# Kernel tuning notes

Measured on AMD Instinct MI355X. Metric: run time of the kernel, lower is better.

The kernel has to match this reference:

```python
import jax, jax.numpy as jnp
import numpy as np

B, S, D = 4, 1024, 1024
H = 16
DK = D // H  # 64
F = 4096
EPS = 1e-6


def layer_norm(x, gamma, beta):
    mu = jnp.mean(x, axis=-1, keepdims=True)
    var = jnp.mean(jnp.square(x - mu), axis=-1, keepdims=True)
    return (x - mu) * jax.lax.rsqrt(var + EPS) * gamma + beta


def setup_inputs() -> dict:
    key = jax.random.key(0)
    ks = jax.random.split(key, 16)
    sd = 0.02
    return {
        "x": jax.random.normal(ks[0], (B, S, D), dtype=jnp.float32),
        "Wq": jax.random.normal(ks[1], (H, D, DK), dtype=jnp.float32) * sd,
        "bq": jnp.zeros((H, DK), dtype=jnp.float32),
        "Wk": jax.random.normal(ks[2], (H, D, DK), dtype=jnp.float32) * sd,
        "bk": jnp.zeros((H, DK), dtype=jnp.float32),
        "Wv": jax.random.normal(ks[3], (H, D, DK), dtype=jnp.float32) * sd,
        "bv": jnp.zeros((H, DK), dtype=jnp.float32),
        "Wo": jax.random.normal(ks[4], (D, D), dtype=jnp.float32) * sd,
        "bo": jnp.zeros((D,), dtype=jnp.float32),
        "W1": jax.random.normal(ks[5], (D, F), dtype=jnp.float32) * sd,
        "b1": jnp.zeros((F,), dtype=jnp.float32),
        "W2": jax.random.normal(ks[6], (F, D), dtype=jnp.float32) * sd,
        "b2": jnp.zeros((D,), dtype=jnp.float32),
        "g1": jnp.ones((D,), dtype=jnp.float32),
        "be1": jnp.zeros((D,), dtype=jnp.float32),
        "g2": jnp.ones((D,), dtype=jnp.float32),
        "be2": jnp.zeros((D,), dtype=jnp.float32),
    }


def reference(x, Wq, bq, Wk, bk, Wv, bv, Wo, bo, W1, b1, W2, b2, g1, be1, g2, be2):
    # Per-head Dense projections, expressed as one batched einsum.
    # q/k/v: [B, H, S, DK]
    q = jnp.einsum('bsd,hdk->bhsk', x, Wq) + bq[:, None, :]
    k = jnp.einsum('bsd,hdk->bhsk', x, Wk) + bk[:, None, :]
    v = jnp.einsum('bsd,hdk->bhsk', x, Wv) + bv[:, None, :]
    scale = 1.0 / jnp.sqrt(jnp.float32(DK))
    scores = jnp.einsum('bhqk,bhsk->bhqs', q, k) * scale  # [B,H,S,S]
    attn = jax.nn.softmax(scores, axis=-1)
    ctx = jnp.einsum('bhqs,bhsk->bhqk', attn, v)  # [B,H,S,DK]
    # concat heads along last dim -> [B,S,D]
    ctx = jnp.transpose(ctx, (0, 2, 1, 3)).reshape(B, S, D)
    mh = ctx @ Wo + bo
    # dropout is identity at inference
    h1 = layer_norm(mh + x, g1, be1)
    ffn = jax.nn.relu(h1 @ W1 + b1) @ W2 + b2
    out = layer_norm(h1 + ffn, g2, be2)
    return out
```

## Files before the change

### kernel.cpp

```cpp
#include <hip/hip_runtime.h>
#include <hip/hip_bf16.h>
#include <stdint.h>


typedef __bf16 bf16x8 __attribute__((ext_vector_type(8)));
typedef float f32x4 __attribute__((ext_vector_type(4)));

__device__ __forceinline__ f32x4 mfma16(bf16x8 a, bf16x8 b, f32x4 c) {
  return __builtin_amdgcn_mfma_f32_16x16x32_bf16(a, b, c, 0, 0, 0);
}

__device__ __forceinline__ void gload_lds16(const void* g, void* l) {
  typedef const unsigned int __attribute__((address_space(1)))* GP;
  typedef unsigned int __attribute__((address_space(3)))* LP;
  __builtin_amdgcn_global_load_lds((GP)(uintptr_t)g,
                                   (LP)(unsigned int)(uintptr_t)l, 16, 0, 0);
}

template <int EPI>
__global__ __launch_bounds__(256, 2) void gemm_bt(
    const __bf16* __restrict__ A, const __bf16* __restrict__ BT,
    const float* __restrict__ bias, float* __restrict__ Cf,
    __bf16* __restrict__ Cb, int M, int N, int K)
{
  __shared__ __attribute__((aligned(16))) __bf16 As[128 * 32];
  __shared__ __attribute__((aligned(16))) __bf16 Bs[128 * 32];
  const int tid = threadIdx.x;
  const int lane = tid & 63;
  const int w = tid >> 6;
  const int wr = w >> 1, wc = w & 1;
  const int l15 = lane & 15, lhi = lane >> 4;
  const int m0 = blockIdx.y * 128, n0 = blockIdx.x * 128;

  const f32x4 fz = {0.f, 0.f, 0.f, 0.f};
  f32x4 acc[4][4];
#pragma unroll
  for (int i = 0; i < 4; i++)
#pragma unroll
    for (int j = 0; j < 4; j++) acc[i][j] = fz;

  const int arow = tid >> 2;
  const int acol = (tid & 3) * 8;
  const __bf16* Ag = A + (long)(m0 + arow) * K + acol;
  const __bf16* Bg = BT + (long)(n0 + arow) * K + acol;
  __bf16* Al = &As[tid * 8];
  __bf16* Bl = &Bs[tid * 8];

  for (int k0 = 0; k0 < K; k0 += 32) {
    gload_lds16(Ag + k0, Al);
    gload_lds16(Ag + k0 + 64 * (long)K, Al + 2048);
    gload_lds16(Bg + k0, Bl);
    gload_lds16(Bg + k0 + 64 * (long)K, Bl + 2048);
    __syncthreads();
    bf16x8 a[4], b[4];
#pragma unroll
    for (int i = 0; i < 4; i++) {
      a[i] = *(const bf16x8*)&As[(wr * 64 + i * 16 + l15) * 32 + lhi * 8];
      b[i] = *(const bf16x8*)&Bs[(wc * 64 + i * 16 + l15) * 32 + lhi * 8];
    }
#pragma unroll
    for (int i = 0; i < 4; i++)
#pragma unroll
      for (int j = 0; j < 4; j++) acc[i][j] = mfma16(a[i], b[j], acc[i][j]);
    __syncthreads();
  }

  if (EPI == 0) {
#pragma unroll
    for (int i = 0; i < 4; i++) {
      const int mB = m0 + wr * 64 + i * 16 + lhi * 4;
#pragma unroll
      for (int j = 0; j < 4; j++) {
        const int n = n0 + wc * 64 + j * 16 + l15;
        const float bs = bias[n];
#pragma unroll
        for (int r = 0; r < 4; r++)
          Cf[(long)(mB + r) * N + n] = acc[i][j][r] + bs;
      }
    }
  } else if (EPI == 1) {
#pragma unroll
    for (int i = 0; i < 4; i++) {
      const int mB = m0 + wr * 64 + i * 16 + lhi * 4;
#pragma unroll
      for (int j = 0; j < 4; j++) {
        const int n = n0 + wc * 64 + j * 16 + l15;
        const float bs = bias[n];
#pragma unroll
        for (int r = 0; r < 4; r++) {
          float v = acc[i][j][r] + bs;
          v = v > 0.f ? v : 0.f;
          Cb[(long)(mB + r) * N + n] = (__bf16)v;
        }
      }
    }
  } else {
#pragma unroll
    for (int i = 0; i < 4; i++) {
      const int mB = m0 + wr * 64 + i * 16 + lhi * 4;
#pragma unroll
      for (int j = 0; j < 4; j++) {
        const int n = n0 + wc * 64 + j * 16 + l15;
        const int proj = n >> 10, h = (n >> 6) & 15, dk = n & 63;
        const float bs = bias[n];
#pragma unroll
        for (int r = 0; r < 4; r++) {
          const int m = mB + r;
          const int b = m >> 10, sidx = m & 1023;
          Cb[(long)proj * 4194304 +
             ((long)(b * 16 + h) * 1024 + sidx) * 64 + dk] =
              (__bf16)(acc[i][j][r] + bs);
        }
      }
    }
  }
}

__global__ __launch_bounds__(256) void vtrans_kernel(
    const __bf16* __restrict__ in, __bf16* __restrict__ out)
{
  __shared__ __bf16 t[64][66];
  const int bh = blockIdx.y, s0 = blockIdx.x * 64;
  const int tx = threadIdx.x & 63, ty = threadIdx.x >> 6;
  const __bf16* ip = in + (long)bh * 65536 + (long)s0 * 64;
  __bf16* op = out + (long)bh * 65536;
#pragma unroll
  for (int i = 0; i < 64; i += 4) t[ty + i][tx] = ip[(ty + i) * 64 + tx];
  __syncthreads();
#pragma unroll
  for (int i = 0; i < 64; i += 4)
    op[(long)(ty + i) * 1024 + s0 + tx] = t[tx][ty + i];
}

__global__ __launch_bounds__(256, 2) void attn_kernel(
    const __bf16* __restrict__ qg_, const __bf16* __restrict__ kg_,
    const __bf16* __restrict__ vtg_, __bf16* __restrict__ ctx)
{
  __shared__ __attribute__((aligned(16))) __bf16 Kb[2][64 * 64];
  __shared__ __attribute__((aligned(16))) __bf16 Vb[2][64 * 64];
  __shared__ __attribute__((aligned(16))) __bf16 Ps[4][16 * 64];
  const int tid = threadIdx.x, lane = tid & 63, w = tid >> 6;
  const int l15 = lane & 15, lhi = lane >> 4;
  const int bh = blockIdx.y;
  const int b = bh >> 4, h = bh & 15;
  const int q0 = blockIdx.x * 64 + w * 16;

  const __bf16* qg = qg_ + ((long)bh * 1024 + q0) * 64;
  const __bf16* kg = kg_ + (long)bh * 65536;
  const __bf16* vtg = vtg_ + (long)bh * 65536;

  bf16x8 qa[2];
  qa[0] = *(const bf16x8*)&qg[l15 * 64 + lhi * 8];
  qa[1] = *(const bf16x8*)&qg[l15 * 64 + 32 + lhi * 8];

  const int srow0 = tid >> 3;
  const int srow1 = srow0 + 32;
  const int sw0 = (tid & 7) ^ (srow0 & 7);
  const int sw1 = (tid & 7) ^ (srow1 & 7);
  const __bf16* kst0 = kg + srow0 * 64 + sw0 * 8;
  const __bf16* kst1 = kg + srow1 * 64 + sw1 * 8;
  const __bf16* vst0 = vtg + srow0 * 1024 + sw0 * 8;
  const __bf16* vst1 = vtg + srow1 * 1024 + sw1 * 8;

  const f32x4 fz = {0.f, 0.f, 0.f, 0.f};
  float mrun[4], lrun[4];
  f32x4 o[4];
#pragma unroll
  for (int r = 0; r < 4; r++) { mrun[r] = -1e30f; lrun[r] = 0.f; }
#pragma unroll
  for (int n = 0; n < 4; n++) o[n] = fz;

  const int e = l15 & 7;
  const int c0 = (lhi ^ e) * 8;
  const int c1 = ((4 | lhi) ^ e) * 8;

  {
    __bf16* kb = &Kb[0][tid * 8];
    __bf16* vb = &Vb[0][tid * 8];
    gload_lds16(kst0, kb);
    gload_lds16(kst1, kb + 2048);
    gload_lds16(vst0, vb);
    gload_lds16(vst1, vb + 2048);
  }

  int cur = 0;
  for (int t = 0; t < 16; ++t) {
    __syncthreads();
    if (t + 1 < 16) {
      __bf16* kb = &Kb[cur ^ 1][tid * 8];
      __bf16* vb = &Vb[cur ^ 1][tid * 8];
      gload_lds16(kst0 + (t + 1) * 4096, kb);
      gload_lds16(kst1 + (t + 1) * 4096, kb + 2048);
      gload_lds16(vst0 + (t + 1) * 64, vb);
      gload_lds16(vst1 + (t + 1) * 64, vb + 2048);
    }

    f32x4 s[4];
#pragma unroll
    for (int n = 0; n < 4; n++) s[n] = fz;
    __builtin_amdgcn_s_setprio(1);
#pragma unroll
    for (int n = 0; n < 4; n++) {
      const int row = (n * 16 + l15) * 64;
      bf16x8 kb0 = *(const bf16x8*)&Kb[cur][row + c0];
      bf16x8 kb1 = *(const bf16x8*)&Kb[cur][row + c1];
      s[n] = mfma16(qa[0], kb0, s[n]);
      s[n] = mfma16(qa[1], kb1, s[n]);
    }
    __builtin_amdgcn_s_setprio(0);

    float alpha[4];
    float p[4][4];
#pragma unroll
    for (int r = 0; r < 4; r++) {
      float mx = -1e30f;
#pragma unroll
      for (int n = 0; n < 4; n++) {
        s[n][r] *= 0.125f;
        mx = fmaxf(mx, s[n][r]);
      }
#pragma unroll
      for (int off = 8; off; off >>= 1) mx = fmaxf(mx, __shfl_xor(mx, off));
      const float mnew = fmaxf(mrun[r], mx);
      alpha[r] = __expf(mrun[r] - mnew);
      float ps = 0.f;
#pragma unroll
      for (int n = 0; n < 4; n++) {
        const float pv = __expf(s[n][r] - mnew);
        p[n][r] = pv;
        ps += pv;
      }
#pragma unroll
      for (int off = 8; off; off >>= 1) ps += __shfl_xor(ps, off);
      mrun[r] = mnew;
      lrun[r] = lrun[r] * alpha[r] + ps;
    }
#pragma unroll
    for (int n = 0; n < 4; n++)
#pragma unroll
      for (int r = 0; r < 4; r++) o[n][r] *= alpha[r];

#pragma unroll
    for (int n = 0; n < 4; n++) {
      const int ch = n * 2 + (l15 >> 3);
#pragma unroll
      for (int r = 0; r < 4; r++) {
        const int row = lhi * 4 + r;
        Ps[w][row * 64 + (ch ^ (row & 7)) * 8 + e] = (__bf16)p[n][r];
      }
    }
    asm volatile("s_waitcnt lgkmcnt(0)" ::: "memory");

    __builtin_amdgcn_s_setprio(1);
#pragma unroll
    for (int kk = 0; kk < 2; kk++) {
      bf16x8 pa = *(const bf16x8*)&Ps[w][l15 * 64 + (kk ? c1 : c0)];
#pragma unroll
      for (int n = 0; n < 4; n++) {
        bf16x8 vb = *(const bf16x8*)&Vb[cur][(n * 16 + l15) * 64 + (kk ? c1 : c0)];
        o[n] = mfma16(pa, vb, o[n]);
      }
    }
    __builtin_amdgcn_s_setprio(0);
    cur ^= 1;
  }

  const long crow = (long)b * 1024 + q0;
#pragma unroll
  for (int n = 0; n < 4; n++)
#pragma unroll
    for (int r = 0; r < 4; r++) {
      const float val = o[n][r] / lrun[r];
      ctx[(crow + lhi * 4 + r) * 1024 + h * 64 + n * 16 + l15] = (__bf16)val;
    }
}

__global__ __launch_bounds__(256) void ln_kernel(
    const float* __restrict__ a, const float* __restrict__ b,
    const float* __restrict__ gamma, const float* __restrict__ beta,
    float* __restrict__ outf, __bf16* __restrict__ outb)
{
  const int row = blockIdx.x;
  const int tid = threadIdx.x;
  const float4 va = ((const float4*)(a + (long)row * 1024))[tid];
  const float4 vb = ((const float4*)(b + (long)row * 1024))[tid];
  const float x0 = va.x + vb.x, x1 = va.y + vb.y, x2 = va.z + vb.z,
              x3 = va.w + vb.w;
  float sum = x0 + x1 + x2 + x3;
  float sq = x0 * x0 + x1 * x1 + x2 * x2 + x3 * x3;
#pragma unroll
  for (int off = 32; off; off >>= 1) {
    sum += __shfl_down(sum, off);
    sq += __shfl_down(sq, off);
  }
  __shared__ float red[8];
  const int w = tid >> 6;
  if ((tid & 63) == 0) { red[w] = sum; red[4 + w] = sq; }
  __syncthreads();
  sum = red[0] + red[1] + red[2] + red[3];
  sq = red[4] + red[5] + red[6] + red[7];
  const float mean = sum * (1.f / 1024.f);
  const float var = sq * (1.f / 1024.f) - mean * mean;
  const float inv = rsqrtf(var + 1e-6f);
  const float4 g = ((const float4*)gamma)[tid];
  const float4 be = ((const float4*)beta)[tid];
  const float y0 = (x0 - mean) * inv * g.x + be.x;
  const float y1 = (x1 - mean) * inv * g.y + be.y;
  const float y2 = (x2 - mean) * inv * g.z + be.z;
  const float y3 = (x3 - mean) * inv * g.w + be.w;
  float4 o4; o4.x = y0; o4.y = y1; o4.z = y2; o4.w = y3;
  ((float4*)(outf + (long)row * 1024))[tid] = o4;
  if (outb) {
    __bf16* ob = outb + (long)row * 1024 + tid * 4;
    ob[0] = (__bf16)y0; ob[1] = (__bf16)y1;
    ob[2] = (__bf16)y2; ob[3] = (__bf16)y3;
  }
}

__global__ __launch_bounds__(256) void cast_bf16_kernel(
    const float* __restrict__ in, __bf16* __restrict__ out, int n4)
{
  const int i = blockIdx.x * 256 + threadIdx.x;
  if (i < n4) {
    const float4 v = ((const float4*)in)[i];
    __bf16* o = out + (long)i * 4;
    o[0] = (__bf16)v.x; o[1] = (__bf16)v.y;
    o[2] = (__bf16)v.z; o[3] = (__bf16)v.w;
  }
}

__global__ __launch_bounds__(256) void pack_bias_kernel(
    const float* __restrict__ bq, const float* __restrict__ bk,
    const float* __restrict__ bv, float* __restrict__ out)
{
  const int i = blockIdx.x * 256 + threadIdx.x;
  if (i < 3072) {
    const float* src = i < 1024 ? bq : (i < 2048 ? bk : bv);
    out[i] = src[i & 1023];
  }
}

__global__ __launch_bounds__(256) void transpose_cast_kernel(
    const float* __restrict__ in, __bf16* __restrict__ out, int R, int C,
    long ibs, long obs)
{
  __shared__ float t[32][33];
  const float* ip = in + (long)blockIdx.z * ibs;
  __bf16* op = out + (long)blockIdx.z * obs;
  const int c0 = blockIdx.x * 32, r0 = blockIdx.y * 32;
  const int tx = threadIdx.x & 31, ty = threadIdx.x >> 5;
#pragma unroll
  for (int i = 0; i < 32; i += 8)
    t[ty + i][tx] = ip[(long)(r0 + ty + i) * C + (c0 + tx)];
  __syncthreads();
#pragma unroll
  for (int i = 0; i < 32; i += 8)
    op[(long)(c0 + ty + i) * R + (r0 + tx)] = (__bf16)t[tx][ty + i];
}

extern "C" void kernel_launch(void* const* d_in, const int* in_sizes, int n_in,
                              void* d_out, int out_size, void* d_ws,
                              size_t ws_size, hipStream_t stream)
{
  const float* x   = (const float*)d_in[0];
  const float* Wq  = (const float*)d_in[1];
  const float* bq  = (const float*)d_in[2];
  const float* Wk  = (const float*)d_in[3];
  const float* bk  = (const float*)d_in[4];
  const float* Wv  = (const float*)d_in[5];
  const float* bv  = (const float*)d_in[6];
  const float* Wo  = (const float*)d_in[7];
  const float* bo  = (const float*)d_in[8];
  const float* W1  = (const float*)d_in[9];
  const float* b1  = (const float*)d_in[10];
  const float* W2  = (const float*)d_in[11];
  const float* b2  = (const float*)d_in[12];
  const float* g1  = (const float*)d_in[13];
  const float* be1 = (const float*)d_in[14];
  const float* g2  = (const float*)d_in[15];
  const float* be2 = (const float*)d_in[16];
  float* out = (float*)d_out;

  char* ws = (char*)d_ws;
  __bf16* wqkvT = (__bf16*)(ws);
  __bf16* woT   = (__bf16*)(ws + 6291456);
  __bf16* w1T   = (__bf16*)(ws + 8388608);
  __bf16* w2T   = (__bf16*)(ws + 16777216);
  float*  bqkv  = (float*)(ws + 25165824);
  __bf16* xbf   = (__bf16*)(ws + 25178112);
  __bf16* ctxb  = xbf;
  __bf16* qkv   = (__bf16*)(ws + 33566720);
  __bf16* h1b   = (__bf16*)(ws + 33566720);
  __bf16* f1b   = (__bf16*)(ws + 41955328);
  float*  h1    = (float*)(ws + 75509760);
  __bf16* vt    = (__bf16*)d_out;
  float*  mh    = out;
  float*  f2    = out;

  cast_bf16_kernel<<<4096, 256, 0, stream>>>(x, xbf, 1048576);
  pack_bias_kernel<<<12, 256, 0, stream>>>(bq, bk, bv, bqkv);
  transpose_cast_kernel<<<dim3(2, 32, 16), 256, 0, stream>>>(
      Wq, wqkvT, 1024, 64, 65536, 65536);
  transpose_cast_kernel<<<dim3(2, 32, 16), 256, 0, stream>>>(
      Wk, wqkvT + 1048576, 1024, 64, 65536, 65536);
  transpose_cast_kernel<<<dim3(2, 32, 16), 256, 0, stream>>>(
      Wv, wqkvT + 2097152, 1024, 64, 65536, 65536);
  transpose_cast_kernel<<<dim3(32, 32, 1), 256, 0, stream>>>(
      Wo, woT, 1024, 1024, 0, 0);
  transpose_cast_kernel<<<dim3(128, 32, 1), 256, 0, stream>>>(
      W1, w1T, 1024, 4096, 0, 0);
  transpose_cast_kernel<<<dim3(32, 128, 1), 256, 0, stream>>>(
      W2, w2T, 4096, 1024, 0, 0);

  gemm_bt<2><<<dim3(24, 32), 256, 0, stream>>>(
      xbf, wqkvT, bqkv, nullptr, qkv, 4096, 3072, 1024);

  vtrans_kernel<<<dim3(16, 64), 256, 0, stream>>>(qkv + 8388608, vt);

  attn_kernel<<<dim3(16, 64), 256, 0, stream>>>(
      qkv, qkv + 4194304, vt, ctxb);

  gemm_bt<0><<<dim3(8, 32), 256, 0, stream>>>(
      ctxb, woT, bo, mh, nullptr, 4096, 1024, 1024);

  ln_kernel<<<4096, 256, 0, stream>>>(mh, x, g1, be1, h1, h1b);

  gemm_bt<1><<<dim3(32, 32), 256, 0, stream>>>(
      h1b, w1T, b1, nullptr, f1b, 4096, 4096, 1024);
  gemm_bt<0><<<dim3(8, 32), 256, 0, stream>>>(
      f1b, w2T, b2, f2, nullptr, 4096, 1024, 4096);

  ln_kernel<<<4096, 256, 0, stream>>>(f2, h1, g2, be2, out, nullptr);
}
```

Baseline: 412.2 us.

## Add 256x256 double-buffered GEMM, split-K for narrow GEMMs, fuse partial sums into LayerNorm

Introduces a 512-thread GEMM kernel with 256x256 tiles, K-step 64, double-buffered LDS fills, an XOR-swizzled LDS layout and grouped block ordering. It is used for the QKV projection and the first FFN matmul. The N=1024 GEMMs (Wo and W2) become a two-way split-K, writing two fp32 partials that the LayerNorm kernels sum together with the residual, so those GEMMs launch more blocks. The second residual is now read from the bf16 copy of h1 rather than a separate fp32 buffer, which saves traffic but slightly lowers precision.

New measurement: 374.9 us. 1.1x faster.

```diff
diff --git a/kernel.cpp b/kernel.cpp
--- a/kernel.cpp
+++ b/kernel.cpp
@@ -4,6 +4,7 @@
 
 
 typedef __bf16 bf16x8 __attribute__((ext_vector_type(8)));
+typedef __bf16 bf16x4 __attribute__((ext_vector_type(4)));
 typedef float f32x4 __attribute__((ext_vector_type(4)));
 
 __device__ __forceinline__ f32x4 mfma16(bf16x8 a, bf16x8 b, f32x4 c) {
@@ -18,10 +19,143 @@
 }
 
 template <int EPI>
-__global__ __launch_bounds__(256, 2) void gemm_bt(
+__global__ __launch_bounds__(512, 2) void gemm256(
     const __bf16* __restrict__ A, const __bf16* __restrict__ BT,
-    const float* __restrict__ bias, float* __restrict__ Cf,
-    __bf16* __restrict__ Cb, int M, int N, int K)
+    const float* __restrict__ bias, __bf16* __restrict__ Cb,
+    int M, int N, int K)
+{
+  __shared__ __attribute__((aligned(16))) __bf16 lds[2][2][2][8192];
+  const int tid = threadIdx.x;
+  const int lane = tid & 63;
+  const int w = tid >> 6;
+  const int l15 = lane & 15, lhi = lane >> 4;
+
+  const int nbx = gridDim.x;
+  const int nwg = nbx * gridDim.y;
+  const int wid = blockIdx.y * nbx + blockIdx.x;
+  const int sw = (wid & 7) * (nwg >> 3) + (wid >> 3);
+  const int n0 = (sw % nbx) * 256;
+  const int m0 = (sw / nbx) * 256;
+
+  const int mat = w >> 2, halfI = (w >> 1) & 1, sub = w & 1;
+  const __bf16* srcM = mat ? BT : A;
+  const long rowG = (long)((mat ? n0 : m0) + halfI * 128 + sub * 64 + (lane >> 3));
+  const __bf16* gsrc =
+      srcM + rowG * K + (((lane & 7) ^ ((lane >> 3) & 7)) << 3);
+  const int ldst = sub * 4096 + lane * 8;
+
+  const int owr = w >> 2, owc = w & 3;
+
+  const f32x4 fz = {0.f, 0.f, 0.f, 0.f};
+  f32x4 acc[8][4];
+#pragma unroll
+  for (int i = 0; i < 8; i++)
+#pragma unroll
+    for (int j = 0; j < 4; j++) acc[i][j] = fz;
+
+  const int KT = K >> 6;
+  const int swz = (l15 & 7);
+
+#pragma unroll
+  for (int i = 0; i < 8; i++)
+    gload_lds16(gsrc + (long)i * 8 * K, &lds[0][mat][halfI][ldst + i * 512]);
+
+  for (int kt = 0; kt < KT; ++kt) {
+    const int buf = kt & 1;
+    if (kt + 1 < KT) {
+#pragma unroll
+      for (int i = 0; i < 8; i++)
+        gload_lds16(gsrc + (long)(kt + 1) * 64 + (long)i * 8 * K,
+                    &lds[buf ^ 1][mat][halfI][ldst + i * 512]);
+      asm volatile("s_waitcnt vmcnt(8)" ::: "memory");
+    } else {
+      asm volatile("s_waitcnt vmcnt(0)" ::: "memory");
+    }
+    __builtin_amdgcn_s_barrier();
+    __builtin_amdgcn_sched_barrier(0);
+
+    const __bf16* Abase = &lds[buf][0][owr][0];
+    const __bf16* Bbase = &lds[buf][1][owc >> 1][0];
+    const int brow0 = (owc & 1) * 64;
+
+    bf16x8 bfr[4][2];
+#pragma unroll
+    for (int nf = 0; nf < 4; nf++)
+#pragma unroll
+      for (int kk = 0; kk < 2; kk++) {
+        const int row = brow0 + nf * 16 + l15;
+        bfr[nf][kk] =
+            *(const bf16x8*)&Bbase[row * 64 + ((((kk << 2) | lhi) ^ swz) << 3)];
+      }
+
+#pragma unroll
+    for (int q = 0; q < 4; q++) {
+      bf16x8 af[2][2];
+#pragma unroll
+      for (int m2 = 0; m2 < 2; m2++)
+#pragma unroll
+        for (int kk = 0; kk < 2; kk++) {
+          const int row = (q * 2 + m2) * 16 + l15;
+          af[m2][kk] =
+              *(const bf16x8*)&Abase[row * 64 + ((((kk << 2) | lhi) ^ swz) << 3)];
+        }
+      __builtin_amdgcn_s_barrier();
+      __builtin_amdgcn_s_setprio(1);
+#pragma unroll
+      for (int m2 = 0; m2 < 2; m2++)
+#pragma unroll
+        for (int nf = 0; nf < 4; nf++)
+#pragma unroll
+          for (int kk = 0; kk < 2; kk++)
+            acc[q * 2 + m2][nf] =
+                mfma16(af[m2][kk], bfr[nf][kk], acc[q * 2 + m2][nf]);
+      __builtin_amdgcn_s_setprio(0);
+      __builtin_amdgcn_s_barrier();
+    }
+  }
+
+  if (EPI == 0) {
+#pragma unroll
+    for (int mi = 0; mi < 8; mi++) {
+      const int mB = m0 + owr * 128 + mi * 16 + lhi * 4;
+#pragma unroll
+      for (int nf = 0; nf < 4; nf++) {
+        const int n = n0 + owc * 64 + nf * 16 + l15;
+        const int proj = n >> 10, hh = (n >> 6) & 15, dk = n & 63;
+        const float bs = bias[n];
+#pragma unroll
+        for (int rr = 0; rr < 4; rr++) {
+          const int m = mB + rr;
+          const int b = m >> 10, sidx = m & 1023;
+          Cb[(long)proj * 4194304 +
+             ((long)(b * 16 + hh) * 1024 + sidx) * 64 + dk] =
+              (__bf16)(acc[mi][nf][rr] + bs);
+        }
+      }
+    }
+  } else {
+#pragma unroll
+    for (int mi = 0; mi < 8; mi++) {
+      const int mB = m0 + owr * 128 + mi * 16 + lhi * 4;
+#pragma unroll
+      for (int nf = 0; nf < 4; nf++) {
+        const int n = n0 + owc * 64 + nf * 16 + l15;
+        const float bs = bias[n];
+#pragma unroll
+        for (int rr = 0; rr < 4; rr++) {
+          float v = acc[mi][nf][rr] + bs;
+          v = v > 0.f ? v : 0.f;
+          Cb[(long)(mB + rr) * N + n] = (__bf16)v;
+        }
+      }
+    }
+  }
+}
+
+__global__ __launch_bounds__(256, 2) void gemm_bt_split(
+    const __bf16* __restrict__ A, const __bf16* __restrict__ BT,
+    const float* __restrict__ bias, float* __restrict__ Cf0,
+    float* __restrict__ Cf1, int M, int N, int ld, int Kh)
 {
   __shared__ __attribute__((aligned(16))) __bf16 As[128 * 32];
   __shared__ __attribute__((aligned(16))) __bf16 Bs[128 * 32];
@@ -31,6 +165,7 @@
   const int wr = w >> 1, wc = w & 1;
   const int l15 = lane & 15, lhi = lane >> 4;
   const int m0 = blockIdx.y * 128, n0 = blockIdx.x * 128;
+  const int z = blockIdx.z;
 
   const f32x4 fz = {0.f, 0.f, 0.f, 0.f};
   f32x4 acc[4][4];
@@ -41,16 +176,16 @@
 
   const int arow = tid >> 2;
   const int acol = (tid & 3) * 8;
-  const __bf16* Ag = A + (long)(m0 + arow) * K + acol;
-  const __bf16* Bg = BT + (long)(n0 + arow) * K + acol;
+  const __bf16* Ag = A + (long)(m0 + arow) * ld + z * Kh + acol;
+  const __bf16* Bg = BT + (long)(n0 + arow) * ld + z * Kh + acol;
   __bf16* Al = &As[tid * 8];
   __bf16* Bl = &Bs[tid * 8];
 
-  for (int k0 = 0; k0 < K; k0 += 32) {
+  for (int k0 = 0; k0 < Kh; k0 += 32) {
     gload_lds16(Ag + k0, Al);
-    gload_lds16(Ag + k0 + 64 * (long)K, Al + 2048);
+    gload_lds16(Ag + k0 + 64 * (long)ld, Al + 2048);
     gload_lds16(Bg + k0, Bl);
-    gload_lds16(Bg + k0 + 64 * (long)K, Bl + 2048);
+    gload_lds16(Bg + k0 + 64 * (long)ld, Bl + 2048);
     __syncthreads();
     bf16x8 a[4], b[4];
 #pragma unroll
@@ -65,53 +200,17 @@
     __syncthreads();
   }
 
-  if (EPI == 0) {
-#pragma unroll
-    for (int i = 0; i < 4; i++) {
-      const int mB = m0 + wr * 64 + i * 16 + lhi * 4;
-#pragma unroll
-      for (int j = 0; j < 4; j++) {
-        const int n = n0 + wc * 64 + j * 16 + l15;
-        const float bs = bias[n];
-#pragma unroll
-        for (int r = 0; r < 4; r++)
-          Cf[(long)(mB + r) * N + n] = acc[i][j][r] + bs;
-      }
-    }
-  } else if (EPI == 1) {
-#pragma unroll
-    for (int i = 0; i < 4; i++) {
-      const int mB = m0 + wr * 64 + i * 16 + lhi * 4;
-#pragma unroll
-      for (int j = 0; j < 4; j++) {
-        const int n = n0 + wc * 64 + j * 16 + l15;
-        const float bs = bias[n];
-#pragma unroll
-        for (int r = 0; r < 4; r++) {
-          float v = acc[i][j][r] + bs;
-          v = v > 0.f ? v : 0.f;
-          Cb[(long)(mB + r) * N + n] = (__bf16)v;
-        }
-      }
-    }
-  } else {
-#pragma unroll
-    for (int i = 0; i < 4; i++) {
-      const int mB = m0 + wr * 64 + i * 16 + lhi * 4;
-#pragma unroll
-      for (int j = 0; j < 4; j++) {
-        const int n = n0 + wc * 64 + j * 16 + l15;
-        const int proj = n >> 10, h = (n >> 6) & 15, dk = n & 63;
-        const float bs = bias[n];
-#pragma unroll
-        for (int r = 0; r < 4; r++) {
-          const int m = mB + r;
-          const int b = m >> 10, sidx = m & 1023;
-          Cb[(long)proj * 4194304 +
-             ((long)(b * 16 + h) * 1024 + sidx) * 64 + dk] =
-              (__bf16)(acc[i][j][r] + bs);
-        }
-      }
+  float* Cf = z ? Cf1 : Cf0;
+#pragma unroll
+  for (int i = 0; i < 4; i++) {
+    const int mB = m0 + wr * 64 + i * 16 + lhi * 4;
+#pragma unroll
+    for (int j = 0; j < 4; j++) {
+      const int n = n0 + wc * 64 + j * 16 + l15;
+      const float bs = z ? 0.f : bias[n];
+#pragma unroll
+      for (int r = 0; r < 4; r++)
+        Cf[(long)(mB + r) * N + n] = acc[i][j][r] + bs;
     }
   }
 }
@@ -257,7 +356,8 @@
       bf16x8 pa = *(const bf16x8*)&Ps[w][l15 * 64 + (kk ? c1 : c0)];
 #pragma unroll
       for (int n = 0; n < 4; n++) {
-        bf16x8 vb = *(const bf16x8*)&Vb[cur][(n * 16 + l15) * 64 + (kk ? c1 : c0)];
+        bf16x8 vb =
+            *(const bf16x8*)&Vb[cur][(n * 16 + l15) * 64 + (kk ? c1 : c0)];
         o[n] = mfma16(pa, vb, o[n]);
       }
     }
@@ -275,17 +375,28 @@
     }
 }
 
-__global__ __launch_bounds__(256) void ln_kernel(
+template <int CB, int OB>
+__global__ __launch_bounds__(256) void ln_fuse3(
     const float* __restrict__ a, const float* __restrict__ b,
-    const float* __restrict__ gamma, const float* __restrict__ beta,
-    float* __restrict__ outf, __bf16* __restrict__ outb)
+    const void* __restrict__ c_, const float* __restrict__ gamma,
+    const float* __restrict__ beta, float* __restrict__ outf,
+    __bf16* __restrict__ outb)
 {
   const int row = blockIdx.x;
   const int tid = threadIdx.x;
   const float4 va = ((const float4*)(a + (long)row * 1024))[tid];
   const float4 vb = ((const float4*)(b + (long)row * 1024))[tid];
-  const float x0 = va.x + vb.x, x1 = va.y + vb.y, x2 = va.z + vb.z,
-              x3 = va.w + vb.w;
+  float c0, c1, c2, c3;
+  if (CB) {
+    const bf16x4 cv =
+        *(const bf16x4*)((const __bf16*)c_ + (long)row * 1024 + tid * 4);
+    c0 = (float)cv[0]; c1 = (float)cv[1]; c2 = (float)cv[2]; c3 = (float)cv[3];
+  } else {
+    const float4 vc = ((const float4*)((const float*)c_ + (long)row * 1024))[tid];
+    c0 = vc.x; c1 = vc.y; c2 = vc.z; c3 = vc.w;
+  }
+  const float x0 = va.x + vb.x + c0, x1 = va.y + vb.y + c1,
+              x2 = va.z + vb.z + c2, x3 = va.w + vb.w + c3;
   float sum = x0 + x1 + x2 + x3;
   float sq = x0 * x0 + x1 * x1 + x2 * x2 + x3 * x3;
 #pragma unroll
@@ -308,12 +419,13 @@
   const float y1 = (x1 - mean) * inv * g.y + be.y;
   const float y2 = (x2 - mean) * inv * g.z + be.z;
   const float y3 = (x3 - mean) * inv * g.w + be.w;
-  float4 o4; o4.x = y0; o4.y = y1; o4.z = y2; o4.w = y3;
-  ((float4*)(outf + (long)row * 1024))[tid] = o4;
-  if (outb) {
+  if (OB) {
     __bf16* ob = outb + (long)row * 1024 + tid * 4;
     ob[0] = (__bf16)y0; ob[1] = (__bf16)y1;
     ob[2] = (__bf16)y2; ob[3] = (__bf16)y3;
+  } else {
+    float4 o4; o4.x = y0; o4.y = y1; o4.z = y2; o4.w = y3;
+    ((float4*)(outf + (long)row * 1024))[tid] = o4;
   }
 }
 
@@ -390,12 +502,13 @@
   __bf16* xbf   = (__bf16*)(ws + 25178112);
   __bf16* ctxb  = xbf;
   __bf16* qkv   = (__bf16*)(ws + 33566720);
-  __bf16* h1b   = (__bf16*)(ws + 33566720);
-  __bf16* f1b   = (__bf16*)(ws + 41955328);
-  float*  h1    = (float*)(ws + 75509760);
+  float*  mh_p1 = (float*)(ws + 33566720);
+  __bf16* h1b   = (__bf16*)(ws + 50343936);
+  __bf16* f1b   = (__bf16*)(ws + 58732544);
+  float*  f2_p1 = (float*)(ws + 25178112);
   __bf16* vt    = (__bf16*)d_out;
-  float*  mh    = out;
-  float*  f2    = out;
+  float*  mh_p0 = out;
+  float*  f2_p0 = out;
 
   cast_bf16_kernel<<<4096, 256, 0, stream>>>(x, xbf, 1048576);
   pack_bias_kernel<<<12, 256, 0, stream>>>(bq, bk, bv, bqkv);
@@ -412,23 +525,26 @@
   transpose_cast_kernel<<<dim3(32, 128, 1), 256, 0, stream>>>(
       W2, w2T, 4096, 1024, 0, 0);
 
-  gemm_bt<2><<<dim3(24, 32), 256, 0, stream>>>(
-      xbf, wqkvT, bqkv, nullptr, qkv, 4096, 3072, 1024);
+  gemm256<0><<<dim3(12, 16), 512, 0, stream>>>(
+      xbf, wqkvT, bqkv, qkv, 4096, 3072, 1024);
 
   vtrans_kernel<<<dim3(16, 64), 256, 0, stream>>>(qkv + 8388608, vt);
 
   attn_kernel<<<dim3(16, 64), 256, 0, stream>>>(
       qkv, qkv + 4194304, vt, ctxb);
 
-  gemm_bt<0><<<dim3(8, 32), 256, 0, stream>>>(
-      ctxb, woT, bo, mh, nullptr, 4096, 1024, 1024);
-
-  ln_kernel<<<4096, 256, 0, stream>>>(mh, x, g1, be1, h1, h1b);
-
-  gemm_bt<1><<<dim3(32, 32), 256, 0, stream>>>(
-      h1b, w1T, b1, nullptr, f1b, 4096, 4096, 1024);
-  gemm_bt<0><<<dim3(8, 32), 256, 0, stream>>>(
-      f1b, w2T, b2, f2, nullptr, 4096, 1024, 4096);
-
-  ln_kernel<<<4096, 256, 0, stream>>>(f2, h1, g2, be2, out, nullptr);
-}
+  gemm_bt_split<<<dim3(8, 32, 2), 256, 0, stream>>>(
+      ctxb, woT, bo, mh_p0, mh_p1, 4096, 1024, 1024, 512);
+
+  ln_fuse3<0, 1><<<4096, 256, 0, stream>>>(
+      mh_p0, mh_p1, x, g1, be1, nullptr, h1b);
+
+  gemm256<1><<<dim3(16, 16), 512, 0, stream>>>(
+      h1b, w1T, b1, f1b, 4096, 4096, 1024);
+
+  gemm_bt_split<<<dim3(8, 32, 2), 256, 0, stream>>>(
+      f1b, w2T, b2, f2_p0, f2_p1, 4096, 1024, 4096, 2048);
+
+  ln_fuse3<1, 0><<<4096, 256, 0, stream>>>(
+      f2_p0, f2_p1, h1b, g2, be2, out, nullptr);
+}
```
